# Performance work log

Measured on AMD Instinct MI355X. Metric: run time of the kernel, lower is better.

Reference implementation:

```python
import jax, jax.numpy as jnp
import numpy as np

B, NX, NY = 16, 1024, 1024


def _grad(f, axis):
    # torch.gradient(f, dim=axis, edge_order=2), unit spacing
    fm = jnp.moveaxis(f, axis, -1)
    g = (jnp.roll(fm, -1, -1) - jnp.roll(fm, 1, -1)) * 0.5
    g0 = (-3.0 * fm[..., 0] + 4.0 * fm[..., 1] - fm[..., 2]) * 0.5
    gN = (3.0 * fm[..., -1] - 4.0 * fm[..., -2] + fm[..., -3]) * 0.5
    g = g.at[..., 0].set(g0).at[..., -1].set(gN)
    return jnp.moveaxis(g, -1, axis)


def _grad2(f, axis):
    # roll-based second derivative with one-sided 2nd-order boundary stencils
    fm = jnp.moveaxis(f, axis, -1)
    g = jnp.roll(fm, -1, -1) - 2.0 * fm + jnp.roll(fm, 1, -1)
    g0 = 2.0 * fm[..., 0] - 5.0 * fm[..., 1] + 4.0 * fm[..., 2] - fm[..., 3]
    gN = 2.0 * fm[..., -1] - 5.0 * fm[..., -2] + 4.0 * fm[..., -3] - fm[..., -4]
    g = g.at[..., 0].set(g0).at[..., -1].set(gN)
    return jnp.moveaxis(g, -1, axis)


def setup_inputs() -> dict:
    key = jax.random.key(0)
    k1, k2, k3, k4 = jax.random.split(key, 4)
    f = jax.random.uniform(k1, (B, NX, NY), dtype=jnp.float32)
    A_grid = jax.random.normal(k2, (2, NX, NY), dtype=jnp.float32)
    B_grid = jax.random.uniform(k3, (3, NX, NY), dtype=jnp.float32)
    dt = jax.random.uniform(k4, (B,), dtype=jnp.float32)
    return {"f": f, "A_grid": A_grid, "B_grid": B_grid, "dt": dt}


def reference(f, A_grid, B_grid, dt):
    # Af: [B,2,NX,NY], Bf: [B,3,NX,NY]
    Af = A_grid[None] * f[:, None]
    Bf = B_grid[None] * f[:, None]
    gradv_Af = _grad(Af[:, 0], 1) + _grad(Af[:, 1], 2)
    gradvv_Bf = (
        _grad2(Bf[:, 0], 1)
        + _grad2(Bf[:, 1], 2)
        + _grad(_grad(Bf[:, 2], 2), 1)
        + _grad(_grad(Bf[:, 2], 1), 2)
    )
    df = -gradv_Af + gradvv_Bf * 0.5
    f_new = f + df * dt[:, None, None]
    # ensure_non_negative_f=True
    return jnp.maximum(f_new, 0.0)
```

## Files before the change

kernel.cpp:

```cpp
#include <hip/hip_runtime.h>

#define BATCH 16
#define NX 1024
#define NY 1024
#define CHUNK 16
#define PLANE (NX * NY)

typedef float v4f __attribute__((ext_vector_type(4)));


struct Raw {
    v4f f, a0, a1, b0, b1, b2;
    float fl, a1l, b1l, b2l;
    float fr, a1r, b1r, b2r;
};

struct Row4 { float fc[4], pa[4], rr[4], dq[4], d2s[4], dtT[4]; };

__device__ __forceinline__ Raw load_raw(int xx, int y0, int tid,
    const float* __restrict__ fb, const float* __restrict__ A0,
    const float* __restrict__ A1, const float* __restrict__ B0,
    const float* __restrict__ B1, const float* __restrict__ B2)
{
    const int base = xx * NY + y0;
    Raw r;
    r.f  = *(const v4f*)(fb + base);
    r.a0 = *(const v4f*)(A0 + base);
    r.a1 = *(const v4f*)(A1 + base);
    r.b0 = *(const v4f*)(B0 + base);
    r.b1 = *(const v4f*)(B1 + base);
    r.b2 = *(const v4f*)(B2 + base);

    const int lane = tid & 63;
    const bool nl = (lane == 0)  && (tid > 0);
    const bool nr = (lane == 63) && (tid < 255);
    r.fl  = nl ? fb[base - 1] : 0.0f;
    r.a1l = nl ? A1[base - 1] : 0.0f;
    r.b1l = nl ? B1[base - 1] : 0.0f;
    r.b2l = nl ? B2[base - 1] : 0.0f;
    r.fr  = nr ? fb[base + 4] : 0.0f;
    r.a1r = nr ? A1[base + 4] : 0.0f;
    r.b1r = nr ? B1[base + 4] : 0.0f;
    r.b2r = nr ? B2[base + 4] : 0.0f;
    return r;
}

__device__ __forceinline__ Row4 convert(const Raw& r, int tid)
{
    const int lane = tid & 63;

    const float q0 = r.a1.x * r.f.x, q1 = r.a1.y * r.f.y,
                q2 = r.a1.z * r.f.z, q3 = r.a1.w * r.f.w;
    const float s0 = r.b1.x * r.f.x, s1 = r.b1.y * r.f.y,
                s2 = r.b1.z * r.f.z, s3 = r.b1.w * r.f.w;
    const float t0 = r.b2.x * r.f.x, t1 = r.b2.y * r.f.y,
                t2 = r.b2.z * r.f.z, t3 = r.b2.w * r.f.w;

    float qm = __shfl_up(q3, 1), sm = __shfl_up(s3, 1), tm = __shfl_up(t3, 1);
    float qp = __shfl_down(q0, 1), sp = __shfl_down(s0, 1), tp = __shfl_down(t0, 1);
    if (lane == 0)  { qm = r.a1l * r.fl; sm = r.b1l * r.fl; tm = r.b2l * r.fl; }
    if (lane == 63) { qp = r.a1r * r.fr; sp = r.b1r * r.fr; tp = r.b2r * r.fr; }

    const float qe[6] = { qm, q0, q1, q2, q3, qp };
    const float se[6] = { sm, s0, s1, s2, s3, sp };
    const float te[6] = { tm, t0, t1, t2, t3, tp };

    Row4 o;
    o.fc[0] = r.f.x; o.fc[1] = r.f.y; o.fc[2] = r.f.z; o.fc[3] = r.f.w;
    o.pa[0] = r.a0.x * r.f.x; o.pa[1] = r.a0.y * r.f.y;
    o.pa[2] = r.a0.z * r.f.z; o.pa[3] = r.a0.w * r.f.w;
    o.rr[0] = r.b0.x * r.f.x; o.rr[1] = r.b0.y * r.f.y;
    o.rr[2] = r.b0.z * r.f.z; o.rr[3] = r.b0.w * r.f.w;

    #pragma unroll
    for (int i = 0; i < 4; ++i) {
        o.dq[i]  = 0.5f * (qe[i + 2] - qe[i]);
        o.d2s[i] = se[i + 2] - 2.0f * se[i + 1] + se[i];
        o.dtT[i] = 0.5f * (te[i + 2] - te[i]);
    }
    if (tid == 0) {
        o.dq[0]  = 0.5f * (-3.0f * qe[1] + 4.0f * qe[2] - qe[3]);
        o.d2s[0] = 2.0f * se[1] - 5.0f * se[2] + 4.0f * se[3] - se[4];
        o.dtT[0] = 0.5f * (-3.0f * te[1] + 4.0f * te[2] - te[3]);
    }
    if (tid == 255) {
        o.dq[3]  = 0.5f * (3.0f * qe[4] - 4.0f * qe[3] + qe[2]);
        o.d2s[3] = 2.0f * se[4] - 5.0f * se[3] + 4.0f * se[2] - se[1];
        o.dtT[3] = 0.5f * (3.0f * te[4] - 4.0f * te[3] + te[2]);
    }
    return o;
}

__global__ __launch_bounds__(256) void fp2d_kernel(
    const float* __restrict__ f,
    const float* __restrict__ Ag,
    const float* __restrict__ Bg,
    const float* __restrict__ dt,
    float* __restrict__ out)
{
    const int tid = threadIdx.x;
    const int y0  = tid * 4;
    const int x0  = blockIdx.x * CHUNK;
    const int b   = blockIdx.y;

    const float* __restrict__ fb = f + (size_t)b * PLANE;
    float* __restrict__ ob = out + (size_t)b * PLANE;
    const float dtb = dt[b];
    const float* __restrict__ A0 = Ag;
    const float* __restrict__ A1 = Ag + PLANE;
    const float* __restrict__ B0 = Bg;
    const float* __restrict__ B1 = Bg + PLANE;
    const float* __restrict__ B2 = Bg + 2 * PLANE;

    const int cs = (x0 == 0) ? 1 : x0;
    const int ce = (x0 + CHUNK == NX) ? NX - 2 : x0 + CHUNK - 1;

    Row4 m = convert(load_raw(cs - 1, y0, tid, fb, A0, A1, B0, B1, B2), tid);
    Row4 c = convert(load_raw(cs,     y0, tid, fb, A0, A1, B0, B1, B2), tid);
    Raw rp = load_raw(cs + 1, y0, tid, fb, A0, A1, B0, B1, B2);

    #pragma unroll 2
    for (int x = cs; x <= ce; ++x) {
        const int xn = (x + 2 < NX) ? x + 2 : NX - 1;
        Raw rn = load_raw(xn, y0, tid, fb, A0, A1, B0, B1, B2);
        Row4 p = convert(rp, tid);
        v4f o;
        #pragma unroll
        for (int i = 0; i < 4; ++i) {
            const float dxP   = 0.5f * (p.pa[i] - m.pa[i]);
            const float dxxR  = p.rr[i] - 2.0f * c.rr[i] + m.rr[i];
            const float dxdyT = 0.5f * (p.dtT[i] - m.dtT[i]);
            const float df = -(dxP + c.dq[i]) + 0.5f * (dxxR + c.d2s[i]) + dxdyT;
            o[i] = fmaxf(c.fc[i] + df * dtb, 0.0f);
        }
        __builtin_nontemporal_store(o, (v4f*)(ob + x * NY + y0));
        m = c; c = p; rp = rn;
    }

    if (x0 == 0) {
        Row4 r0 = convert(load_raw(0, y0, tid, fb, A0, A1, B0, B1, B2), tid);
        Row4 r1 = convert(load_raw(1, y0, tid, fb, A0, A1, B0, B1, B2), tid);
        Row4 r2 = convert(load_raw(2, y0, tid, fb, A0, A1, B0, B1, B2), tid);
        Row4 r3 = convert(load_raw(3, y0, tid, fb, A0, A1, B0, B1, B2), tid);
        v4f o;
        #pragma unroll
        for (int i = 0; i < 4; ++i) {
            const float dxP   = 0.5f * (-3.0f * r0.pa[i] + 4.0f * r1.pa[i] - r2.pa[i]);
            const float dxxR  = 2.0f * r0.rr[i] - 5.0f * r1.rr[i] + 4.0f * r2.rr[i] - r3.rr[i];
            const float dxdyT = 0.5f * (-3.0f * r0.dtT[i] + 4.0f * r1.dtT[i] - r2.dtT[i]);
            const float df = -(dxP + r0.dq[i]) + 0.5f * (dxxR + r0.d2s[i]) + dxdyT;
            o[i] = fmaxf(r0.fc[i] + df * dtb, 0.0f);
        }
        __builtin_nontemporal_store(o, (v4f*)(ob + y0));
    }

    if (x0 + CHUNK == NX) {
        Row4 r0 = convert(load_raw(NX - 1, y0, tid, fb, A0, A1, B0, B1, B2), tid);
        Row4 r1 = convert(load_raw(NX - 2, y0, tid, fb, A0, A1, B0, B1, B2), tid);
        Row4 r2 = convert(load_raw(NX - 3, y0, tid, fb, A0, A1, B0, B1, B2), tid);
        Row4 r3 = convert(load_raw(NX - 4, y0, tid, fb, A0, A1, B0, B1, B2), tid);
        v4f o;
        #pragma unroll
        for (int i = 0; i < 4; ++i) {
            const float dxP   = 0.5f * (3.0f * r0.pa[i] - 4.0f * r1.pa[i] + r2.pa[i]);
            const float dxxR  = 2.0f * r0.rr[i] - 5.0f * r1.rr[i] + 4.0f * r2.rr[i] - r3.rr[i];
            const float dxdyT = 0.5f * (3.0f * r0.dtT[i] - 4.0f * r1.dtT[i] + r2.dtT[i]);
            const float df = -(dxP + r0.dq[i]) + 0.5f * (dxxR + r0.d2s[i]) + dxdyT;
            o[i] = fmaxf(r0.fc[i] + df * dtb, 0.0f);
        }
        __builtin_nontemporal_store(o, (v4f*)(ob + (NX - 1) * NY + y0));
    }
}

extern "C" void kernel_launch(void* const* d_in, const int* in_sizes, int n_in,
                              void* d_out, int out_size, void* d_ws, size_t ws_size,
                              hipStream_t stream) {
    const float* f  = (const float*)d_in[0];
    const float* Ag = (const float*)d_in[1];
    const float* Bg = (const float*)d_in[2];
    const float* dt = (const float*)d_in[3];
    float* out = (float*)d_out;

    dim3 block(256, 1, 1);
    dim3 grid(NX / CHUNK, BATCH, 1);
    fp2d_kernel<<<grid, block, 0, stream>>>(f, Ag, Bg, dt, out);
}
```

Measured before the change: 161.7 us.

## Process two batches per block, sharing grid-coefficient loads and halo shuffles

Each block now handles two batch planes. The five coefficient rows (A0, A1, B0, B1, B2) and their lane-boundary shuffles are loaded once and reused for both batches, cutting redundant coefficient loads and shuffle work per output. CHUNK is halved to keep the block count the same, which raises the halo re-read overhead per chunk. The y-direction terms are also pre-combined into a single value per row. Holding more live state per thread raises register pressure and may lower occupancy.

```diff
diff --git a/kernel.cpp b/kernel.cpp
--- a/kernel.cpp
+++ b/kernel.cpp
@@ -3,90 +3,109 @@
 #define BATCH 16
 #define NX 1024
 #define NY 1024
-#define CHUNK 16
+#define CHUNK 8
+#define NB 2
 #define PLANE (NX * NY)
 
 typedef float v4f __attribute__((ext_vector_type(4)));
 
-
-struct Raw {
-    v4f f, a0, a1, b0, b1, b2;
-    float fl, a1l, b1l, b2l;
-    float fr, a1r, b1r, b2r;
-};
-
-struct Row4 { float fc[4], pa[4], rr[4], dq[4], d2s[4], dtT[4]; };
-
-__device__ __forceinline__ Raw load_raw(int xx, int y0, int tid,
-    const float* __restrict__ fb, const float* __restrict__ A0,
-    const float* __restrict__ A1, const float* __restrict__ B0,
-    const float* __restrict__ B1, const float* __restrict__ B2)
+struct RawS { v4f a0, a1, b0, b1, b2; float a1l, b1l, b2l, a1r, b1r, b2r; };
+struct RawF { v4f f; float fl, fr; };
+struct Halo { float a1m, b1m, b2m, a1p, b1p, b2p; };
+struct Row  { float pa[4], rr[4], tt[4], fc[4], yc[4]; };
+
+__device__ __forceinline__ RawS load_rawS(int xx, int y0, int tid,
+    const float* __restrict__ A0, const float* __restrict__ A1,
+    const float* __restrict__ B0, const float* __restrict__ B1,
+    const float* __restrict__ B2)
 {
     const int base = xx * NY + y0;
-    Raw r;
-    r.f  = *(const v4f*)(fb + base);
+    RawS r;
     r.a0 = *(const v4f*)(A0 + base);
     r.a1 = *(const v4f*)(A1 + base);
     r.b0 = *(const v4f*)(B0 + base);
     r.b1 = *(const v4f*)(B1 + base);
     r.b2 = *(const v4f*)(B2 + base);
-
     const int lane = tid & 63;
     const bool nl = (lane == 0)  && (tid > 0);
     const bool nr = (lane == 63) && (tid < 255);
-    r.fl  = nl ? fb[base - 1] : 0.0f;
     r.a1l = nl ? A1[base - 1] : 0.0f;
     r.b1l = nl ? B1[base - 1] : 0.0f;
     r.b2l = nl ? B2[base - 1] : 0.0f;
-    r.fr  = nr ? fb[base + 4] : 0.0f;
     r.a1r = nr ? A1[base + 4] : 0.0f;
     r.b1r = nr ? B1[base + 4] : 0.0f;
     r.b2r = nr ? B2[base + 4] : 0.0f;
     return r;
 }
 
-__device__ __forceinline__ Row4 convert(const Raw& r, int tid)
-{
-    const int lane = tid & 63;
-
-    const float q0 = r.a1.x * r.f.x, q1 = r.a1.y * r.f.y,
-                q2 = r.a1.z * r.f.z, q3 = r.a1.w * r.f.w;
-    const float s0 = r.b1.x * r.f.x, s1 = r.b1.y * r.f.y,
-                s2 = r.b1.z * r.f.z, s3 = r.b1.w * r.f.w;
-    const float t0 = r.b2.x * r.f.x, t1 = r.b2.y * r.f.y,
-                t2 = r.b2.z * r.f.z, t3 = r.b2.w * r.f.w;
-
-    float qm = __shfl_up(q3, 1), sm = __shfl_up(s3, 1), tm = __shfl_up(t3, 1);
-    float qp = __shfl_down(q0, 1), sp = __shfl_down(s0, 1), tp = __shfl_down(t0, 1);
-    if (lane == 0)  { qm = r.a1l * r.fl; sm = r.b1l * r.fl; tm = r.b2l * r.fl; }
-    if (lane == 63) { qp = r.a1r * r.fr; sp = r.b1r * r.fr; tp = r.b2r * r.fr; }
-
-    const float qe[6] = { qm, q0, q1, q2, q3, qp };
-    const float se[6] = { sm, s0, s1, s2, s3, sp };
-    const float te[6] = { tm, t0, t1, t2, t3, tp };
-
-    Row4 o;
-    o.fc[0] = r.f.x; o.fc[1] = r.f.y; o.fc[2] = r.f.z; o.fc[3] = r.f.w;
-    o.pa[0] = r.a0.x * r.f.x; o.pa[1] = r.a0.y * r.f.y;
-    o.pa[2] = r.a0.z * r.f.z; o.pa[3] = r.a0.w * r.f.w;
-    o.rr[0] = r.b0.x * r.f.x; o.rr[1] = r.b0.y * r.f.y;
-    o.rr[2] = r.b0.z * r.f.z; o.rr[3] = r.b0.w * r.f.w;
+__device__ __forceinline__ RawF load_rawF(int xx, int y0, int tid,
+    const float* __restrict__ fb)
+{
+    const int base = xx * NY + y0;
+    RawF r;
+    r.f = *(const v4f*)(fb + base);
+    const int lane = tid & 63;
+    const bool nl = (lane == 0)  && (tid > 0);
+    const bool nr = (lane == 63) && (tid < 255);
+    r.fl = nl ? fb[base - 1] : 0.0f;
+    r.fr = nr ? fb[base + 4] : 0.0f;
+    return r;
+}
+
+__device__ __forceinline__ Halo make_halo(const RawS& rs, int tid)
+{
+    const int lane = tid & 63;
+    Halo h;
+    h.a1m = __shfl_up(rs.a1.w, 1);   h.b1m = __shfl_up(rs.b1.w, 1);
+    h.b2m = __shfl_up(rs.b2.w, 1);
+    h.a1p = __shfl_down(rs.a1.x, 1); h.b1p = __shfl_down(rs.b1.x, 1);
+    h.b2p = __shfl_down(rs.b2.x, 1);
+    if (lane == 0)  { h.a1m = rs.a1l; h.b1m = rs.b1l; h.b2m = rs.b2l; }
+    if (lane == 63) { h.a1p = rs.a1r; h.b1p = rs.b1r; h.b2p = rs.b2r; }
+    return h;
+}
+
+__device__ __forceinline__ Row convert(const RawS& rs, const Halo& h,
+                                       const RawF& rf, int tid)
+{
+    const int lane = tid & 63;
+    float fm = __shfl_up(rf.f.w, 1);
+    float fp = __shfl_down(rf.f.x, 1);
+    if (lane == 0)  fm = rf.fl;
+    if (lane == 63) fp = rf.fr;
+
+    const float qe[6] = { h.a1m * fm, rs.a1.x * rf.f.x, rs.a1.y * rf.f.y,
+                          rs.a1.z * rf.f.z, rs.a1.w * rf.f.w, h.a1p * fp };
+    const float se[6] = { h.b1m * fm, rs.b1.x * rf.f.x, rs.b1.y * rf.f.y,
+                          rs.b1.z * rf.f.z, rs.b1.w * rf.f.w, h.b1p * fp };
+    const float te[6] = { h.b2m * fm, rs.b2.x * rf.f.x, rs.b2.y * rf.f.y,
+                          rs.b2.z * rf.f.z, rs.b2.w * rf.f.w, h.b2p * fp };
+
+    Row o;
+    o.fc[0] = rf.f.x; o.fc[1] = rf.f.y; o.fc[2] = rf.f.z; o.fc[3] = rf.f.w;
+    o.pa[0] = rs.a0.x * rf.f.x; o.pa[1] = rs.a0.y * rf.f.y;
+    o.pa[2] = rs.a0.z * rf.f.z; o.pa[3] = rs.a0.w * rf.f.w;
+    o.rr[0] = rs.b0.x * rf.f.x; o.rr[1] = rs.b0.y * rf.f.y;
+    o.rr[2] = rs.b0.z * rf.f.z; o.rr[3] = rs.b0.w * rf.f.w;
 
     #pragma unroll
     for (int i = 0; i < 4; ++i) {
-        o.dq[i]  = 0.5f * (qe[i + 2] - qe[i]);
-        o.d2s[i] = se[i + 2] - 2.0f * se[i + 1] + se[i];
-        o.dtT[i] = 0.5f * (te[i + 2] - te[i]);
+        const float dq  = 0.5f * (qe[i + 2] - qe[i]);
+        const float d2s = se[i + 2] - 2.0f * se[i + 1] + se[i];
+        o.tt[i] = 0.5f * (te[i + 2] - te[i]);
+        o.yc[i] = -dq + 0.5f * d2s;
     }
     if (tid == 0) {
-        o.dq[0]  = 0.5f * (-3.0f * qe[1] + 4.0f * qe[2] - qe[3]);
-        o.d2s[0] = 2.0f * se[1] - 5.0f * se[2] + 4.0f * se[3] - se[4];
-        o.dtT[0] = 0.5f * (-3.0f * te[1] + 4.0f * te[2] - te[3]);
+        const float dq  = 0.5f * (-3.0f * qe[1] + 4.0f * qe[2] - qe[3]);
+        const float d2s = 2.0f * se[1] - 5.0f * se[2] + 4.0f * se[3] - se[4];
+        o.tt[0] = 0.5f * (-3.0f * te[1] + 4.0f * te[2] - te[3]);
+        o.yc[0] = -dq + 0.5f * d2s;
     }
     if (tid == 255) {
-        o.dq[3]  = 0.5f * (3.0f * qe[4] - 4.0f * qe[3] + qe[2]);
-        o.d2s[3] = 2.0f * se[4] - 5.0f * se[3] + 4.0f * se[2] - se[1];
-        o.dtT[3] = 0.5f * (3.0f * te[4] - 4.0f * te[3] + te[2]);
+        const float dq  = 0.5f * (3.0f * qe[4] - 4.0f * qe[3] + qe[2]);
+        const float d2s = 2.0f * se[4] - 5.0f * se[3] + 4.0f * se[2] - se[1];
+        o.tt[3] = 0.5f * (3.0f * te[4] - 4.0f * te[3] + te[2]);
+        o.yc[3] = -dq + 0.5f * d2s;
     }
     return o;
 }
@@ -101,74 +120,126 @@
     const int tid = threadIdx.x;
     const int y0  = tid * 4;
     const int x0  = blockIdx.x * CHUNK;
-    const int b   = blockIdx.y;
-
-    const float* __restrict__ fb = f + (size_t)b * PLANE;
-    float* __restrict__ ob = out + (size_t)b * PLANE;
-    const float dtb = dt[b];
+    const int bb  = blockIdx.y * NB;
+
     const float* __restrict__ A0 = Ag;
     const float* __restrict__ A1 = Ag + PLANE;
     const float* __restrict__ B0 = Bg;
     const float* __restrict__ B1 = Bg + PLANE;
     const float* __restrict__ B2 = Bg + 2 * PLANE;
 
+    const float* fb[NB];
+    float* ob[NB];
+    float dtb[NB];
+    #pragma unroll
+    for (int j = 0; j < NB; ++j) {
+        fb[j]  = f   + (size_t)(bb + j) * PLANE;
+        ob[j]  = out + (size_t)(bb + j) * PLANE;
+        dtb[j] = dt[bb + j];
+    }
+
     const int cs = (x0 == 0) ? 1 : x0;
     const int ce = (x0 + CHUNK == NX) ? NX - 2 : x0 + CHUNK - 1;
 
-    Row4 m = convert(load_raw(cs - 1, y0, tid, fb, A0, A1, B0, B1, B2), tid);
-    Row4 c = convert(load_raw(cs,     y0, tid, fb, A0, A1, B0, B1, B2), tid);
-    Raw rp = load_raw(cs + 1, y0, tid, fb, A0, A1, B0, B1, B2);
-
-    #pragma unroll 2
+    {
+    }
+    RawS sM = load_rawS(cs - 1, y0, tid, A0, A1, B0, B1, B2);
+    RawS sC = load_rawS(cs,     y0, tid, A0, A1, B0, B1, B2);
+    RawS sP = load_rawS(cs + 1, y0, tid, A0, A1, B0, B1, B2);
+    RawF fM[NB], fC[NB], fP[NB];
+    #pragma unroll
+    for (int j = 0; j < NB; ++j) {
+        fM[j] = load_rawF(cs - 1, y0, tid, fb[j]);
+        fC[j] = load_rawF(cs,     y0, tid, fb[j]);
+        fP[j] = load_rawF(cs + 1, y0, tid, fb[j]);
+    }
+    Halo hM = make_halo(sM, tid);
+    Halo hC = make_halo(sC, tid);
+    Row m[NB], c[NB];
+    #pragma unroll
+    for (int j = 0; j < NB; ++j) {
+        m[j] = convert(sM, hM, fM[j], tid);
+        c[j] = convert(sC, hC, fC[j], tid);
+    }
+
     for (int x = cs; x <= ce; ++x) {
         const int xn = (x + 2 < NX) ? x + 2 : NX - 1;
-        Raw rn = load_raw(xn, y0, tid, fb, A0, A1, B0, B1, B2);
-        Row4 p = convert(rp, tid);
-        v4f o;
-        #pragma unroll
-        for (int i = 0; i < 4; ++i) {
-            const float dxP   = 0.5f * (p.pa[i] - m.pa[i]);
-            const float dxxR  = p.rr[i] - 2.0f * c.rr[i] + m.rr[i];
-            const float dxdyT = 0.5f * (p.dtT[i] - m.dtT[i]);
-            const float df = -(dxP + c.dq[i]) + 0.5f * (dxxR + c.d2s[i]) + dxdyT;
-            o[i] = fmaxf(c.fc[i] + df * dtb, 0.0f);
+        RawS sN = load_rawS(xn, y0, tid, A0, A1, B0, B1, B2);
+        RawF fN[NB];
+        #pragma unroll
+        for (int j = 0; j < NB; ++j) fN[j] = load_rawF(xn, y0, tid, fb[j]);
+
+        Halo hP = make_halo(sP, tid);
+        #pragma unroll
+        for (int j = 0; j < NB; ++j) {
+            Row p = convert(sP, hP, fP[j], tid);
+            v4f o;
+            #pragma unroll
+            for (int i = 0; i < 4; ++i) {
+                const float dxP   = 0.5f * (p.pa[i] - m[j].pa[i]);
+                const float dxxR  = p.rr[i] - 2.0f * c[j].rr[i] + m[j].rr[i];
+                const float dxdyT = 0.5f * (p.tt[i] - m[j].tt[i]);
+                const float df = -dxP + c[j].yc[i] + 0.5f * dxxR + dxdyT;
+                o[i] = fmaxf(c[j].fc[i] + df * dtb[j], 0.0f);
+            }
+            __builtin_nontemporal_store(o, (v4f*)(ob[j] + x * NY + y0));
+            m[j] = c[j]; c[j] = p;
         }
-        __builtin_nontemporal_store(o, (v4f*)(ob + x * NY + y0));
-        m = c; c = p; rp = rn;
+        sP = sN;
+        #pragma unroll
+        for (int j = 0; j < NB; ++j) fP[j] = fN[j];
     }
 
     if (x0 == 0) {
-        Row4 r0 = convert(load_raw(0, y0, tid, fb, A0, A1, B0, B1, B2), tid);
-        Row4 r1 = convert(load_raw(1, y0, tid, fb, A0, A1, B0, B1, B2), tid);
-        Row4 r2 = convert(load_raw(2, y0, tid, fb, A0, A1, B0, B1, B2), tid);
-        Row4 r3 = convert(load_raw(3, y0, tid, fb, A0, A1, B0, B1, B2), tid);
-        v4f o;
-        #pragma unroll
-        for (int i = 0; i < 4; ++i) {
-            const float dxP   = 0.5f * (-3.0f * r0.pa[i] + 4.0f * r1.pa[i] - r2.pa[i]);
-            const float dxxR  = 2.0f * r0.rr[i] - 5.0f * r1.rr[i] + 4.0f * r2.rr[i] - r3.rr[i];
-            const float dxdyT = 0.5f * (-3.0f * r0.dtT[i] + 4.0f * r1.dtT[i] - r2.dtT[i]);
-            const float df = -(dxP + r0.dq[i]) + 0.5f * (dxxR + r0.d2s[i]) + dxdyT;
-            o[i] = fmaxf(r0.fc[i] + df * dtb, 0.0f);
+        RawS s0 = load_rawS(0, y0, tid, A0, A1, B0, B1, B2);
+        RawS s1 = load_rawS(1, y0, tid, A0, A1, B0, B1, B2);
+        RawS s2 = load_rawS(2, y0, tid, A0, A1, B0, B1, B2);
+        RawS s3 = load_rawS(3, y0, tid, A0, A1, B0, B1, B2);
+        Halo h0 = make_halo(s0, tid), h1 = make_halo(s1, tid);
+        Halo h2 = make_halo(s2, tid), h3 = make_halo(s3, tid);
+        #pragma unroll
+        for (int j = 0; j < NB; ++j) {
+            Row r0 = convert(s0, h0, load_rawF(0, y0, tid, fb[j]), tid);
+            Row r1 = convert(s1, h1, load_rawF(1, y0, tid, fb[j]), tid);
+            Row r2 = convert(s2, h2, load_rawF(2, y0, tid, fb[j]), tid);
+            Row r3 = convert(s3, h3, load_rawF(3, y0, tid, fb[j]), tid);
+            v4f o;
+            #pragma unroll
+            for (int i = 0; i < 4; ++i) {
+                const float dxP   = 0.5f * (-3.0f * r0.pa[i] + 4.0f * r1.pa[i] - r2.pa[i]);
+                const float dxxR  = 2.0f * r0.rr[i] - 5.0f * r1.rr[i] + 4.0f * r2.rr[i] - r3.rr[i];
+                const float dxdyT = 0.5f * (-3.0f * r0.tt[i] + 4.0f * r1.tt[i] - r2.tt[i]);
+                const float df = -dxP + r0.yc[i] + 0.5f * dxxR + dxdyT;
+                o[i] = fmaxf(r0.fc[i] + df * dtb[j], 0.0f);
+            }
+            __builtin_nontemporal_store(o, (v4f*)(ob[j] + y0));
         }
-        __builtin_nontemporal_store(o, (v4f*)(ob + y0));
     }
 
     if (x0 + CHUNK == NX) {
-        Row4 r0 = convert(load_raw(NX - 1, y0, tid, fb, A0, A1, B0, B1, B2), tid);
-        Row4 r1 = convert(load_raw(NX - 2, y0, tid, fb, A0, A1, B0, B1, B2), tid);
-        Row4 r2 = convert(load_raw(NX - 3, y0, tid, fb, A0, A1, B0, B1, B2), tid);
-        Row4 r3 = convert(load_raw(NX - 4, y0, tid, fb, A0, A1, B0, B1, B2), tid);
-        v4f o;
-        #pragma unroll
-        for (int i = 0; i < 4; ++i) {
-            const float dxP   = 0.5f * (3.0f * r0.pa[i] - 4.0f * r1.pa[i] + r2.pa[i]);
-            const float dxxR  = 2.0f * r0.rr[i] - 5.0f * r1.rr[i] + 4.0f * r2.rr[i] - r3.rr[i];
-            const float dxdyT = 0.5f * (3.0f * r0.dtT[i] - 4.0f * r1.dtT[i] + r2.dtT[i]);
-            const float df = -(dxP + r0.dq[i]) + 0.5f * (dxxR + r0.d2s[i]) + dxdyT;
-            o[i] = fmaxf(r0.fc[i] + df * dtb, 0.0f);
+        RawS s0 = load_rawS(NX - 1, y0, tid, A0, A1, B0, B1, B2);
+        RawS s1 = load_rawS(NX - 2, y0, tid, A0, A1, B0, B1, B2);
+        RawS s2 = load_rawS(NX - 3, y0, tid, A0, A1, B0, B1, B2);
+        RawS s3 = load_rawS(NX - 4, y0, tid, A0, A1, B0, B1, B2);
+        Halo h0 = make_halo(s0, tid), h1 = make_halo(s1, tid);
+        Halo h2 = make_halo(s2, tid), h3 = make_halo(s3, tid);
+        #pragma unroll
+        for (int j = 0; j < NB; ++j) {
+            Row r0 = convert(s0, h0, load_rawF(NX - 1, y0, tid, fb[j]), tid);
+            Row r1 = convert(s1, h1, load_rawF(NX - 2, y0, tid, fb[j]), tid);
+            Row r2 = convert(s2, h2, load_rawF(NX - 3, y0, tid, fb[j]), tid);
+            Row r3 = convert(s3, h3, load_rawF(NX - 4, y0, tid, fb[j]), tid);
+            v4f o;
+            #pragma unroll
+            for (int i = 0; i < 4; ++i) {
+                const float dxP   = 0.5f * (3.0f * r0.pa[i] - 4.0f * r1.pa[i] + r2.pa[i]);
+                const float dxxR  = 2.0f * r0.rr[i] - 5.0f * r1.rr[i] + 4.0f * r2.rr[i] - r3.rr[i];
+                const float dxdyT = 0.5f * (3.0f * r0.tt[i] - 4.0f * r1.tt[i] + r2.tt[i]);
+                const float df = -dxP + r0.yc[i] + 0.5f * dxxR + dxdyT;
+                o[i] = fmaxf(r0.fc[i] + df * dtb[j], 0.0f);
+            }
+            __builtin_nontemporal_store(o, (v4f*)(ob[j] + (NX - 1) * NY + y0));
         }
-        __builtin_nontemporal_store(o, (v4f*)(ob + (NX - 1) * NY + y0));
     }
 }
 
@@ -182,6 +253,6 @@
     float* out = (float*)d_out;
 
     dim3 block(256, 1, 1);
-    dim3 grid(NX / CHUNK, BATCH, 1);
+    dim3 grid(NX / CHUNK, BATCH / NB, 1);
     fp2d_kernel<<<grid, block, 0, stream>>>(f, Ag, Bg, dt, out);
 }
```

Measured after the change: 148.1 us. 8.4% less time.
